# Kernel tuning notes

Measured on AMD Instinct MI355X. Metric: run time of the kernel, lower is better.

## Reference

```python
import jax, jax.numpy as jnp
import numpy as np

B, IN_DIM, HID = 8192, 1024, 1024

def setup_inputs() -> dict:
    key = jax.random.key(0)
    ks = jax.random.split(key, 11)
    s_in = 1.0 / np.sqrt(IN_DIM + HID)  # torch Linear default init scale
    inp = {
        "Z": jax.random.normal(ks[0], (B, IN_DIM), dtype=jnp.float32),
        "h_prev": jax.random.normal(ks[1], (B, HID), dtype=jnp.float32),
        "c_prev": jax.random.normal(ks[2], (B, HID), dtype=jnp.float32),
        "W_i": jax.random.uniform(ks[3], (IN_DIM + HID, HID), jnp.float32, -s_in, s_in),
        "b_i": jax.random.uniform(ks[4], (HID,), jnp.float32, -s_in, s_in),
        "W_f": jax.random.uniform(ks[5], (IN_DIM + HID, HID), jnp.float32, -s_in, s_in),
        "b_f": jax.random.uniform(ks[6], (HID,), jnp.float32, -s_in, s_in),
        "W_o": jax.random.uniform(ks[7], (IN_DIM + HID, HID), jnp.float32, -s_in, s_in),
        "b_o": jax.random.uniform(ks[8], (HID,), jnp.float32, -s_in, s_in),
        "W_g": jax.random.uniform(ks[9], (IN_DIM + HID, HID), jnp.float32, -s_in, s_in),
        "b_g": jax.random.uniform(ks[10], (HID,), jnp.float32, -s_in, s_in),
    }
    return inp

def reference(Z, h_prev, c_prev, W_i, b_i, W_f, b_f, W_o, b_o, W_g, b_g):
    combined = jnp.concatenate([Z, h_prev], axis=1)  # [B, IN+HID]
    i = jax.nn.sigmoid(combined @ W_i + b_i)
    f = jax.nn.sigmoid(combined @ W_f + b_f)
    o = jax.nn.sigmoid(combined @ W_o + b_o)
    g = jnp.tanh(combined @ W_g + b_g)
    c = f * c_prev + i * g
    h = o * jnp.tanh(c)
    return (h, c)
```

## Files before the change

kernel.cpp:

```cpp
#include <hip/hip_runtime.h>


#define BDIM 8192
#define KDIM 2048
#define NDIM 1024
#define NCAT 4096

typedef __bf16 bf16x8 __attribute__((ext_vector_type(8)));
typedef __bf16 bf16x4 __attribute__((ext_vector_type(4)));
typedef float  f32x4  __attribute__((ext_vector_type(4)));

__device__ __forceinline__ void async_cp16(const void* g, void* l) {
    __builtin_amdgcn_global_load_lds((__attribute__((address_space(1))) void*)g,
                                     (__attribute__((address_space(3))) void*)l,
                                     16, 0, 0);
}

__device__ __forceinline__ float sigm(float x) { return 1.f / (1.f + __expf(-x)); }
__device__ __forceinline__ float tanh_fast(float x) { return 1.f - 2.f / (1.f + __expf(2.f * x)); }

__global__ __launch_bounds__(256)
void prep_kernel(const float* __restrict__ Z, const float* __restrict__ H,
                 const float* __restrict__ Wi, const float* __restrict__ Wf,
                 const float* __restrict__ Wo, const float* __restrict__ Wg,
                 __bf16* __restrict__ A, __bf16* __restrict__ Wt) {
    __shared__ float t[64][65];
    const int bid = blockIdx.x;
    const int tid = threadIdx.x;

    if (bid < 8192) {
        const bool isZ = (bid < 4096);
        const int idx  = (isZ ? bid : bid - 4096) * 256 + tid;
        const int row  = idx >> 7;
        const int q8   = idx & 127;
        const float* src = isZ ? Z : H;
        const float4* p = (const float4*)src + ((size_t)row << 8) + q8 * 2;
        float4 v0 = p[0], v1 = p[1];
        bf16x8 o = { (__bf16)v0.x, (__bf16)v0.y, (__bf16)v0.z, (__bf16)v0.w,
                     (__bf16)v1.x, (__bf16)v1.y, (__bf16)v1.z, (__bf16)v1.w };
        const int col8 = isZ ? q8 : (q8 + 128);
        ((bf16x8*)A)[(size_t)row * 256 + col8] = o;
    } else {
        const int id  = bid - 8192;
        const int g   = id >> 9;
        const int rem = id & 511;
        const int k0  = (rem & 31) * 64;
        const int n0  = (rem >> 5) * 64;
        const float* W = (g == 0) ? Wi : (g == 1) ? Wf : (g == 2) ? Wo : Wg;

        const int c4 = tid & 15, r0 = tid >> 4;
        #pragma unroll
        for (int it = 0; it < 4; ++it) {
            const int r = r0 + it * 16;
            float4 v = ((const float4*)W)[(size_t)(k0 + r) * 256 + (n0 >> 2) + c4];
            t[r][c4 * 4 + 0] = v.x;
            t[r][c4 * 4 + 1] = v.y;
            t[r][c4 * 4 + 2] = v.z;
            t[r][c4 * 4 + 3] = v.w;
        }
        __syncthreads();

        const int kc = tid & 7, nn0 = tid >> 3;
        #pragma unroll
        for (int j = 0; j < 2; ++j) {
            const int n    = nn0 + j * 32;
            const int ncat = n0 + n;
            const size_t outRow = (size_t)(ncat >> 5) * 128 + g * 32 + (ncat & 31);
            bf16x8 o;
            #pragma unroll
            for (int kk = 0; kk < 8; ++kk) o[kk] = (__bf16)t[kc * 8 + kk][n];
            *(bf16x8*)(Wt + outRow * KDIM + k0 + kc * 8) = o;
        }
    }
}

__global__ __launch_bounds__(256, 4)
void lstm_gemm_kernel(const __bf16* __restrict__ A, const __bf16* __restrict__ Wt,
                      const float* __restrict__ b_i, const float* __restrict__ b_f,
                      const float* __restrict__ b_o, const float* __restrict__ b_g,
                      const float* __restrict__ c_prev, float* __restrict__ out) {
    __shared__ char smem[32768];
    __bf16* As = (__bf16*)smem;
    __bf16* Bs = (__bf16*)(smem + 16384);
    float*  Ep = (float*)smem;

    const int tid  = threadIdx.x;
    const int wave = tid >> 6;
    const int lane = tid & 63;
    const int wr = wave >> 1, wc = wave & 1;

    const int bid = blockIdx.x;
    const int bx = (bid & 7) * 4 + ((bid >> 3) & 3);
    const int by = bid >> 5;
    const int m0 = by * 128;
    const int ncat0 = bx * 128;

    const int srow   = lane >> 2;
    const int schunk = (lane & 3) ^ ((lane >> 3) & 3);
    const __bf16* Ag[2]; __bf16* Al[2];
    const __bf16* Bg[2]; __bf16* Bl[2];
    #pragma unroll
    for (int i = 0; i < 2; ++i) {
        int grp = wave * 2 + i;
        Ag[i] = A  + (size_t)(m0    + grp * 16 + srow) * KDIM + schunk * 8;
        Bg[i] = Wt + (size_t)(ncat0 + grp * 16 + srow) * KDIM + schunk * 8;
        Al[i] = As + grp * 512;
        Bl[i] = Bs + grp * 512;
    }

    const int l15  = lane & 15;
    const int quad = lane >> 4;
    const int ksw  = (quad ^ ((l15 >> 1) & 3)) * 8;
    int aoff[4], boff[4];
    #pragma unroll
    for (int t = 0; t < 4; ++t) {
        aoff[t] = (wr * 64 + t * 16 + l15) * 32 + ksw;
        boff[t] = (wc * 64 + t * 16 + l15) * 32 + ksw;
    }

    f32x4 acc[4][4];
    #pragma unroll
    for (int i = 0; i < 4; ++i)
        #pragma unroll
        for (int j = 0; j < 4; ++j) acc[i][j] = (f32x4){0.f, 0.f, 0.f, 0.f};

    for (int k0 = 0; k0 < KDIM; k0 += 64) {
        #pragma unroll
        for (int h = 0; h < 2; ++h)
            #pragma unroll
            for (int i = 0; i < 2; ++i) {
                async_cp16(Ag[i] + k0 + h * 32, Al[i] + h * 4096);
                async_cp16(Bg[i] + k0 + h * 32, Bl[i] + h * 4096);
            }
        __syncthreads();

        #pragma unroll
        for (int h = 0; h < 2; ++h) {
            bf16x8 af[4], bfr[4];
            #pragma unroll
            for (int t = 0; t < 4; ++t) af[t]  = *(const bf16x8*)(As + h * 4096 + aoff[t]);
            #pragma unroll
            for (int t = 0; t < 4; ++t) bfr[t] = *(const bf16x8*)(Bs + h * 4096 + boff[t]);
            #pragma unroll
            for (int mt = 0; mt < 4; ++mt)
                #pragma unroll
                for (int nt = 0; nt < 4; ++nt)
                    acc[mt][nt] = __builtin_amdgcn_mfma_f32_16x16x32_bf16(af[mt], bfr[nt], acc[mt][nt], 0, 0, 0);
        }
        __syncthreads();
    }

    const float* bias_lo = (wc == 0) ? b_i : b_o;
    const float* bias_hi = (wc == 0) ? b_f : b_g;
    float bv[4];
    bv[0] = bias_lo[bx * 32 + l15];
    bv[1] = bias_lo[bx * 32 + 16 + l15];
    bv[2] = bias_hi[bx * 32 + l15];
    bv[3] = bias_hi[bx * 32 + 16 + l15];

    #pragma unroll
    for (int c = 0; c < 4; ++c) {
        __syncthreads();
        if (wr == (c >> 1)) {
            #pragma unroll
            for (int mi = 0; mi < 2; ++mi) {
                int mt = (c & 1) * 2 + mi;
                #pragma unroll
                for (int nt = 0; nt < 4; ++nt)
                    #pragma unroll
                    for (int r = 0; r < 4; ++r)
                        Ep[(mi * 16 + quad * 4 + r) * 132 + wc * 64 + nt * 16 + l15] =
                            acc[mt][nt][r] + bv[nt];
            }
        }
        __syncthreads();

        #pragma unroll
        for (int e = 0; e < 4; ++e) {
            int idx = tid + e * 256;
            int row = idx >> 5, n = idx & 31;
            float gi = sigm(Ep[row * 132 + n]);
            float gf = sigm(Ep[row * 132 + 32 + n]);
            float go = sigm(Ep[row * 132 + 64 + n]);
            float gg = tanh_fast(Ep[row * 132 + 96 + n]);
            size_t pos = (size_t)(m0 + c * 32 + row) * NDIM + bx * 32 + n;
            float cp = c_prev[pos];
            float cv = gf * cp + gi * gg;
            out[pos] = go * tanh_fast(cv);
            out[(size_t)BDIM * NDIM + pos] = cv;
        }
    }
}

extern "C" void kernel_launch(void* const* d_in, const int* in_sizes, int n_in,
                              void* d_out, int out_size, void* d_ws, size_t ws_size,
                              hipStream_t stream) {
    const float* Z  = (const float*)d_in[0];
    const float* H  = (const float*)d_in[1];
    const float* Cp = (const float*)d_in[2];
    const float* Wi = (const float*)d_in[3];
    const float* bi = (const float*)d_in[4];
    const float* Wf = (const float*)d_in[5];
    const float* bf = (const float*)d_in[6];
    const float* Wo = (const float*)d_in[7];
    const float* bo = (const float*)d_in[8];
    const float* Wg = (const float*)d_in[9];
    const float* bg = (const float*)d_in[10];

    __bf16* Acomb = (__bf16*)d_ws;
    __bf16* Wt    = (__bf16*)((char*)d_ws + (size_t)33554432);

    prep_kernel<<<10240, 256, 0, stream>>>(Z, H, Wi, Wf, Wo, Wg, Acomb, Wt);
    lstm_gemm_kernel<<<dim3(NCAT / 128 * BDIM / 128), 256, 0, stream>>>(
        Acomb, Wt, bi, bf, bo, bg, Cp, (float*)d_out);
}
```

Measured before the change: 333.4 us.

## Rewrite LSTM GEMM as 256x256 tile, 8-wave double-buffered pipelined kernel

Replaces the 128x128 single-buffered GEMM tile with a 256x256 tile computed by 512 threads (8 waves). The K-loop is double-buffered in 128KB dynamic LDS with staged async global->LDS copies interleaved between quarter-tile MFMA phases, raw s_barrier with explicit waitcnts, and setprio around MFMA. It aims to raise arithmetic intensity and overlap memory loads with matrix math. The cost is lower occupancy, heavy LDS use, and fragile hand-written synchronization. The epilogue is reworked for the new tile layout.

```diff
diff --git a/kernel.cpp b/kernel.cpp
--- a/kernel.cpp
+++ b/kernel.cpp
@@ -5,6 +5,7 @@
 #define KDIM 2048
 #define NDIM 1024
 #define NCAT 4096
+#define NT   32
 
 typedef __bf16 bf16x8 __attribute__((ext_vector_type(8)));
 typedef __bf16 bf16x4 __attribute__((ext_vector_type(4)));
@@ -18,6 +19,8 @@
 
 __device__ __forceinline__ float sigm(float x) { return 1.f / (1.f + __expf(-x)); }
 __device__ __forceinline__ float tanh_fast(float x) { return 1.f - 2.f / (1.f + __expf(2.f * x)); }
+
+#define BARM asm volatile("s_barrier" ::: "memory")
 
 __global__ __launch_bounds__(256)
 void prep_kernel(const float* __restrict__ Z, const float* __restrict__ H,
@@ -74,122 +77,154 @@
     }
 }
 
-__global__ __launch_bounds__(256, 4)
+__global__ __launch_bounds__(512, 2)
 void lstm_gemm_kernel(const __bf16* __restrict__ A, const __bf16* __restrict__ Wt,
                       const float* __restrict__ b_i, const float* __restrict__ b_f,
                       const float* __restrict__ b_o, const float* __restrict__ b_g,
                       const float* __restrict__ c_prev, float* __restrict__ out) {
-    __shared__ char smem[32768];
-    __bf16* As = (__bf16*)smem;
-    __bf16* Bs = (__bf16*)(smem + 16384);
-    float*  Ep = (float*)smem;
+    extern __shared__ char smem[];
 
     const int tid  = threadIdx.x;
     const int wave = tid >> 6;
     const int lane = tid & 63;
-    const int wr = wave >> 1, wc = wave & 1;
-
-    const int bid = blockIdx.x;
-    const int bx = (bid & 7) * 4 + ((bid >> 3) & 3);
-    const int by = bid >> 5;
-    const int m0 = by * 128;
-    const int ncat0 = bx * 128;
-
-    const int srow   = lane >> 2;
-    const int schunk = (lane & 3) ^ ((lane >> 3) & 3);
-    const __bf16* Ag[2]; __bf16* Al[2];
-    const __bf16* Bg[2]; __bf16* Bl[2];
-    #pragma unroll
-    for (int i = 0; i < 2; ++i) {
-        int grp = wave * 2 + i;
-        Ag[i] = A  + (size_t)(m0    + grp * 16 + srow) * KDIM + schunk * 8;
-        Bg[i] = Wt + (size_t)(ncat0 + grp * 16 + srow) * KDIM + schunk * 8;
-        Al[i] = As + grp * 512;
-        Bl[i] = Bs + grp * 512;
-    }
-
+    const int wm   = wave >> 2;
+    const int wn   = wave & 3;
     const int l15  = lane & 15;
     const int quad = lane >> 4;
-    const int ksw  = (quad ^ ((l15 >> 1) & 3)) * 8;
-    int aoff[4], boff[4];
+
+    const int bid = blockIdx.x;
+    const int bxc = (bid & 7) * 2 + (bid >> 8);
+    const int by  = (bid >> 3) & 31;
+    const int m0   = by * 256;
+    const int cat0 = bxc * 256;
+    const int n0   = bxc * 64;
+
+    const int grow   = wave * 8 + (lane >> 3);
+    const int schunk = (lane & 7) ^ (((lane >> 5) & 1) << 1);
+    const __bf16* Ags = A  + (size_t)(m0   + grow) * KDIM + schunk * 8;
+    const __bf16* Bgs = Wt + (size_t)(cat0 + grow) * KDIM + schunk * 8;
+    char* ldsw = smem + wave * 1024;
+
+#define STG(o, h, kt, b) do { \
+    const __bf16* gp_ = ((o) ? Bgs : Ags) + (size_t)(h) * 128 * KDIM + (size_t)(kt) * 64; \
+    char* lp_ = ldsw + (b) * 65536 + (o) * 32768 + (h) * 16384; \
+    async_cp16(gp_, lp_); \
+    async_cp16(gp_ + (size_t)64 * KDIM, lp_ + 8192); \
+} while (0)
+
+    const int xorr = ((l15 >> 2) & 1) << 1;
+    const int cA0  = (quad ^ xorr) * 16;
+    const int cA1  = ((quad + 4) ^ xorr) * 16;
+    const int aoff0 = wm * 16384 + l15 * 128;
+    const int boff0 = 32768 + (wn >> 1) * 16384 + ((wn & 1) * 64 + l15) * 128;
+
+    f32x4 acc[8][4];
     #pragma unroll
-    for (int t = 0; t < 4; ++t) {
-        aoff[t] = (wr * 64 + t * 16 + l15) * 32 + ksw;
-        boff[t] = (wc * 64 + t * 16 + l15) * 32 + ksw;
-    }
-
-    f32x4 acc[4][4];
+    for (int i = 0; i < 8; ++i)
+        #pragma unroll
+        for (int j = 0; j < 4; ++j) acc[i][j] = (f32x4){0.f, 0.f, 0.f, 0.f};
+
+    bf16x8 af[4][2];
+    bf16x8 bf[4][2];
+
+    auto LDA = [&](int mh, int bufb) {
+        const char* p = smem + bufb + aoff0 + mh * 8192;
+        #pragma unroll
+        for (int m = 0; m < 4; ++m) {
+            af[m][0] = *(const bf16x8*)(p + m * 2048 + cA0);
+            af[m][1] = *(const bf16x8*)(p + m * 2048 + cA1);
+        }
+    };
+    auto LDB = [&](int nh, int bufb) {
+        const char* p = smem + bufb + boff0 + nh * 4096;
+        #pragma unroll
+        for (int n = 0; n < 2; ++n) {
+            bf[nh * 2 + n][0] = *(const bf16x8*)(p + n * 2048 + cA0);
+            bf[nh * 2 + n][1] = *(const bf16x8*)(p + n * 2048 + cA1);
+        }
+    };
+    auto MMA = [&](int mh, int nh) {
+        #pragma unroll
+        for (int m = 0; m < 4; ++m)
+            #pragma unroll
+            for (int n = 0; n < 2; ++n) {
+                acc[mh * 4 + m][nh * 2 + n] = __builtin_amdgcn_mfma_f32_16x16x32_bf16(
+                    af[m][0], bf[nh * 2 + n][0], acc[mh * 4 + m][nh * 2 + n], 0, 0, 0);
+                acc[mh * 4 + m][nh * 2 + n] = __builtin_amdgcn_mfma_f32_16x16x32_bf16(
+                    af[m][1], bf[nh * 2 + n][1], acc[mh * 4 + m][nh * 2 + n], 0, 0, 0);
+            }
+    };
+
+    STG(0, 0, 0, 0); STG(1, 0, 0, 0); STG(0, 1, 0, 0); STG(1, 1, 0, 0);
+    STG(0, 0, 1, 1); STG(1, 0, 1, 1);
+    asm volatile("s_waitcnt vmcnt(4)" ::: "memory");
+    BARM;
+
+    #pragma unroll 2
+    for (int t = 0; t < NT; ++t) {
+        const int b    = t & 1;
+        const int bufb = b * 65536;
+        LDA(0, bufb); LDB(0, bufb);
+        if (t + 1 < NT) STG(0, 1, t + 1, b ^ 1);
+        BARM; asm volatile("s_waitcnt lgkmcnt(0)" ::: "memory");
+        __builtin_amdgcn_s_setprio(1); MMA(0, 0); __builtin_amdgcn_s_setprio(0);
+        BARM;
+        LDB(1, bufb);
+        if (t + 1 < NT) STG(1, 1, t + 1, b ^ 1);
+        BARM; asm volatile("s_waitcnt lgkmcnt(0)" ::: "memory");
+        __builtin_amdgcn_s_setprio(1); MMA(0, 1); __builtin_amdgcn_s_setprio(0);
+        BARM;
+        LDA(1, bufb);
+        BARM; asm volatile("s_waitcnt lgkmcnt(0)" ::: "memory");
+        __builtin_amdgcn_s_setprio(1); MMA(1, 0); __builtin_amdgcn_s_setprio(0);
+        BARM;
+        if (t + 2 < NT) { STG(0, 0, t + 2, b); STG(1, 0, t + 2, b); }
+        if (t < NT - 2) { asm volatile("s_waitcnt vmcnt(4)" ::: "memory"); }
+        else            { asm volatile("s_waitcnt vmcnt(0)" ::: "memory"); }
+        BARM;
+        __builtin_amdgcn_s_setprio(1); MMA(1, 1); __builtin_amdgcn_s_setprio(0);
+        BARM;
+    }
+
+    float* Ep = (float*)smem;
+    const int nn = tid & 63;
+    const float bvi = b_i[n0 + nn], bvf = b_f[n0 + nn];
+    const float bvo = b_o[n0 + nn], bvg = b_g[n0 + nn];
+    int colW[4];
     #pragma unroll
-    for (int i = 0; i < 4; ++i)
-        #pragma unroll
-        for (int j = 0; j < 4; ++j) acc[i][j] = (f32x4){0.f, 0.f, 0.f, 0.f};
-
-    for (int k0 = 0; k0 < KDIM; k0 += 64) {
-        #pragma unroll
-        for (int h = 0; h < 2; ++h)
+    for (int nt = 0; nt < 4; ++nt)
+        colW[nt] = ((wn & 1) * 2 + (nt >> 1)) * 64 + (wn >> 1) * 32 + (nt & 1) * 16 + l15;
+
+    #pragma unroll
+    for (int ch = 0; ch < 4; ++ch) {
+        BARM;
+        if (wm == (ch >> 1)) {
             #pragma unroll
-            for (int i = 0; i < 2; ++i) {
-                async_cp16(Ag[i] + k0 + h * 32, Al[i] + h * 4096);
-                async_cp16(Bg[i] + k0 + h * 32, Bl[i] + h * 4096);
-            }
-        __syncthreads();
-
-        #pragma unroll
-        for (int h = 0; h < 2; ++h) {
-            bf16x8 af[4], bfr[4];
-            #pragma unroll
-            for (int t = 0; t < 4; ++t) af[t]  = *(const bf16x8*)(As + h * 4096 + aoff[t]);
-            #pragma unroll
-            for (int t = 0; t < 4; ++t) bfr[t] = *(const bf16x8*)(Bs + h * 4096 + boff[t]);
-            #pragma unroll
-            for (int mt = 0; mt < 4; ++mt)
-                #pragma unroll
-                for (int nt = 0; nt < 4; ++nt)
-                    acc[mt][nt] = __builtin_amdgcn_mfma_f32_16x16x32_bf16(af[mt], bfr[nt], acc[mt][nt], 0, 0, 0);
-        }
-        __syncthreads();
-    }
-
-    const float* bias_lo = (wc == 0) ? b_i : b_o;
-    const float* bias_hi = (wc == 0) ? b_f : b_g;
-    float bv[4];
-    bv[0] = bias_lo[bx * 32 + l15];
-    bv[1] = bias_lo[bx * 32 + 16 + l15];
-    bv[2] = bias_hi[bx * 32 + l15];
-    bv[3] = bias_hi[bx * 32 + 16 + l15];
-
-    #pragma unroll
-    for (int c = 0; c < 4; ++c) {
-        __syncthreads();
-        if (wr == (c >> 1)) {
-            #pragma unroll
-            for (int mi = 0; mi < 2; ++mi) {
-                int mt = (c & 1) * 2 + mi;
+            for (int mi = 0; mi < 4; ++mi) {
+                const int mt = (ch & 1) * 4 + mi;
                 #pragma unroll
                 for (int nt = 0; nt < 4; ++nt)
                     #pragma unroll
                     for (int r = 0; r < 4; ++r)
-                        Ep[(mi * 16 + quad * 4 + r) * 132 + wc * 64 + nt * 16 + l15] =
-                            acc[mt][nt][r] + bv[nt];
+                        Ep[(mi * 16 + quad * 4 + r) * 258 + colW[nt]] = acc[mt][nt][r];
             }
         }
-        __syncthreads();
-
-        #pragma unroll
-        for (int e = 0; e < 4; ++e) {
-            int idx = tid + e * 256;
-            int row = idx >> 5, n = idx & 31;
-            float gi = sigm(Ep[row * 132 + n]);
-            float gf = sigm(Ep[row * 132 + 32 + n]);
-            float go = sigm(Ep[row * 132 + 64 + n]);
-            float gg = tanh_fast(Ep[row * 132 + 96 + n]);
-            size_t pos = (size_t)(m0 + c * 32 + row) * NDIM + bx * 32 + n;
-            float cp = c_prev[pos];
-            float cv = gf * cp + gi * gg;
+        BARM;
+        #pragma unroll
+        for (int e = 0; e < 8; ++e) {
+            const int row = e * 8 + wave;
+            const float gi = sigm(Ep[row * 258 + nn] + bvi);
+            const float gf = sigm(Ep[row * 258 + 64 + nn] + bvf);
+            const float go = sigm(Ep[row * 258 + 128 + nn] + bvo);
+            const float gg = tanh_fast(Ep[row * 258 + 192 + nn] + bvg);
+            const size_t pos = (size_t)(m0 + ch * 64 + row) * NDIM + n0 + nn;
+            const float cp = c_prev[pos];
+            const float cv = gf * cp + gi * gg;
             out[pos] = go * tanh_fast(cv);
             out[(size_t)BDIM * NDIM + pos] = cv;
         }
     }
+#undef STG
 }
 
 extern "C" void kernel_launch(void* const* d_in, const int* in_sizes, int n_in,
@@ -210,7 +245,14 @@
     __bf16* Acomb = (__bf16*)d_ws;
     __bf16* Wt    = (__bf16*)((char*)d_ws + (size_t)33554432);
 
+    static bool cfg = false;
+    if (!cfg) {
+        hipFuncSetAttribute(reinterpret_cast<const void*>(lstm_gemm_kernel),
+                            hipFuncAttributeMaxDynamicSharedMemorySize, 131072);
+        cfg = true;
+    }
+
     prep_kernel<<<10240, 256, 0, stream>>>(Z, H, Wi, Wf, Wo, Wg, Acomb, Wt);
-    lstm_gemm_kernel<<<dim3(NCAT / 128 * BDIM / 128), 256, 0, stream>>>(
+    lstm_gemm_kernel<<<512, 512, 131072, stream>>>(
         Acomb, Wt, bi, bf, bo, bg, Cp, (float*)d_out);
 }
```

Result: faster. 324.8 us (-2.6%).
